# Kernel tuning notes

Measured on AMD Instinct MI355X. Metric: run time of the kernel, lower is better.

## Reference

```python
import jax, jax.numpy as jnp
import numpy as np

B, S, E, H = 2, 1024, 4096, 16
D = E // H          # head_dim = 256
RD = 64             # rotary_dim
# Quantization scales (alpha of the int8 GEMM epilogues)
A_QKV = 1.2e-4      # W8A8B8O8 q/k/v projection output scale
A_QK = 2e-4         # BMM_S8T_S8N_F32T alpha (= q_scale * k_scale)
A_PV = 1.0 / 127.0  # BMM_S8T_S8N_S8T alpha (probs quantized by *127)
A_O = 0.01          # W8A8BFP32OFP32 out_proj alpha


def setup_inputs() -> dict:
    key = jax.random.key(0)
    ks = jax.random.split(key, 9)
    ri = lambda k, shp: jax.random.randint(k, shp, -127, 128).astype(jnp.float32)
    return {
        "hidden_states": ri(ks[0], (B, S, E)),   # int8-valued activations
        "Wq": ri(ks[1], (E, E)),
        "Wk": ri(ks[2], (E, E)),
        "Wv": ri(ks[3], (E, E)),
        "Wo": ri(ks[4], (E, E)),
        "bq": ri(ks[5], (E,)),
        "bk": ri(ks[6], (E,)),
        "bv": ri(ks[7], (E,)),
        "bo": jax.random.normal(ks[8], (E,), dtype=jnp.float32) * 0.02,  # fp32 bias
    }


def _linear_i8(x, W, b, alpha):
    # W8A8B8O8Linear: int8 GEMM, scaled, +int8 bias, round+saturate to int8
    y = alpha * (x @ W.T) + b
    return jnp.clip(jnp.round(y), -128, 127)


def _rotate_every_two(x):
    x1 = x[..., ::2]
    x2 = x[..., 1::2]
    return jnp.stack((-x2, x1), axis=-1).reshape(x.shape)


def _apply_rotary(x, sin, cos):
    # duplicate_interleave == repeat each column twice; broadcast over [B, S, H, rd]
    sin = jnp.repeat(sin, 2, axis=-1)[None, :, None, :]
    cos = jnp.repeat(cos, 2, axis=-1)[None, :, None, :]
    r = x * cos + _rotate_every_two(x) * sin
    # torch: clamp(-128,127).to(int8) -> truncate toward zero
    return jnp.trunc(jnp.clip(r, -128.0, 127.0))


def reference(hidden_states, Wq, Wk, Wv, Wo, bq, bk, bv, bo):
    q = _linear_i8(hidden_states, Wq, bq, A_QKV).reshape(B, S, H, D)
    k = _linear_i8(hidden_states, Wk, bk, A_QKV).reshape(B, S, H, D)
    v = _linear_i8(hidden_states, Wv, bv, A_QKV).reshape(B, S, H, D)
    v = v.transpose(0, 2, 1, 3)  # [B, H, S, D]

    # fixed_pos_embedding over rotary_dim
    inv_freq = 1.0 / (10000.0 ** (jnp.arange(0, RD, 2, dtype=jnp.float32) / RD))
    t = jnp.arange(S, dtype=jnp.float32)
    sinusoid = t[:, None] * inv_freq[None, :]   # [S, RD/2]
    sin, cos = jnp.sin(sinusoid), jnp.cos(sinusoid)

    q = jnp.concatenate([_apply_rotary(q[..., :RD], sin, cos), q[..., RD:]], axis=-1)
    k = jnp.concatenate([_apply_rotary(k[..., :RD], sin, cos), k[..., RD:]], axis=-1)
    q = q.transpose(0, 2, 1, 3)  # [B, H, S, D]
    k = k.transpose(0, 2, 1, 3)

    w = A_QK * jnp.einsum('bhqd,bhkd->bhqk', q, k)
    causal = jnp.tril(jnp.ones((S, S), dtype=bool))[None, None]
    w = jnp.where(causal, w, jnp.finfo(jnp.float32).min)
    w = w / jnp.sqrt(jnp.float32(D))  # scale_attn = sqrt(head_dim)
    p = jnp.round(jax.nn.softmax(w, axis=-1) * 127.0)  # int8-valued probs

    # pv_bmm: int8 probs x int8 values -> scaled, round+saturate to int8
    o = jnp.clip(jnp.round(A_PV * jnp.einsum('bhqk,bhkd->bhqd', p, v)), -128, 127)
    o = o.transpose(0, 2, 1, 3).reshape(B, S, E)  # merge heads

    # out_proj: W8A8BFP32OFP32 -> fp32 output
    return A_O * (o @ Wo.T) + bo
```

## Files before the change

### kernel.cpp

```cpp
#include <hip/hip_runtime.h>
#include <hip/hip_bf16.h>

typedef int int32x4 __attribute__((ext_vector_type(4)));
typedef signed char i8;

#define B_ 2
#define S_ 1024
#define E_ 4096
#define H_ 16
#define D_ 256

#define MFMA_I8(a, b, c) __builtin_amdgcn_mfma_i32_16x16x64_i8((a), (b), (c), 0, 0, 0)

__device__ __forceinline__ int32x4 ld16(const void* p) {
    return *reinterpret_cast<const int32x4*>(p);
}

__device__ __forceinline__ void gload16(const void* g, void* l) {
    __builtin_amdgcn_global_load_lds(
        (const __attribute__((address_space(1))) void*)g,
        (__attribute__((address_space(3))) void*)l, 16, 0, 0);
}

__global__ void k_f32_to_i8(const float* __restrict__ src, i8* __restrict__ dst, int n16) {
    int i = blockIdx.x * blockDim.x + threadIdx.x;
    if (i >= n16) return;
    const float4* s = reinterpret_cast<const float4*>(src) + (size_t)i * 4;
    union { int32x4 v; i8 b[16]; } u;
#pragma unroll
    for (int j = 0; j < 4; ++j) {
        float4 f = s[j];
        u.b[j*4+0] = (i8)f.x; u.b[j*4+1] = (i8)f.y;
        u.b[j*4+2] = (i8)f.z; u.b[j*4+3] = (i8)f.w;
    }
    reinterpret_cast<int32x4*>(dst)[i] = u.v;
}

__global__ void k_sincos(float* __restrict__ sin_t, float* __restrict__ cos_t) {
    int idx = blockIdx.x * blockDim.x + threadIdx.x;
    if (idx >= S_ * 32) return;
    int s = idx >> 5, i = idx & 31;
    float ex = (float)(2 * i) / 64.0f;
    float invf = 1.0f / powf(10000.0f, ex);
    float arg = (float)s * invf;
    sin_t[idx] = (float)sin((double)arg);
    cos_t[idx] = (float)cos((double)arg);
}

template<bool OUT_I8>
__global__ __launch_bounds__(256) void k_gemm_i8(
    const i8* __restrict__ X, const i8* __restrict__ W, const float* __restrict__ bias,
    void* __restrict__ out, float alpha, int M, int N, int K)
{
    __shared__ __align__(16) i8 Alds[128 * 128];
    __shared__ __align__(16) i8 Blds[128 * 128];
    const int m0 = blockIdx.y * 128, n0 = blockIdx.x * 128;
    const int tid = threadIdx.x, lane = tid & 63, wave = tid >> 6;
    const int wr = wave >> 1, wc = wave & 1, l4 = lane & 15, lh = lane >> 4;

    int32x4 acc[4][4];
#pragma unroll
    for (int m = 0; m < 4; ++m)
#pragma unroll
        for (int n = 0; n < 4; ++n) acc[m][n] = int32x4{0, 0, 0, 0};

    for (int k0 = 0; k0 < K; k0 += 128) {
#pragma unroll
        for (int p = 0; p < 4; ++p) {
            int o = wave * 1024 + p * 4096 + lane * 16;
            int row = o >> 7, col = o & 127;
            int lb = wave * 1024 + p * 4096;
            gload16(X + (size_t)(m0 + row) * K + k0 + col, Alds + lb);
            gload16(W + (size_t)(n0 + row) * K + k0 + col, Blds + lb);
        }
        __syncthreads();
#pragma unroll
        for (int kk = 0; kk < 2; ++kk) {
            const int ko = kk * 64 + lh * 16;
            int32x4 a[4], b[4];
#pragma unroll
            for (int i = 0; i < 4; ++i) a[i] = ld16(Alds + (wr * 64 + i * 16 + l4) * 128 + ko);
#pragma unroll
            for (int i = 0; i < 4; ++i) b[i] = ld16(Blds + (wc * 64 + i * 16 + l4) * 128 + ko);
#pragma unroll
            for (int m = 0; m < 4; ++m)
#pragma unroll
                for (int n = 0; n < 4; ++n)
                    acc[m][n] = MFMA_I8(a[m], b[n], acc[m][n]);
        }
        __syncthreads();
    }

#pragma unroll
    for (int m = 0; m < 4; ++m)
#pragma unroll
        for (int n = 0; n < 4; ++n)
#pragma unroll
            for (int r = 0; r < 4; ++r) {
                int grow = m0 + wr * 64 + m * 16 + lh * 4 + r;
                int gcol = n0 + wc * 64 + n * 16 + l4;
                float y = alpha * (float)acc[m][n][r] + bias[gcol];
                if (OUT_I8) {
                    float v = rintf(y);
                    v = fminf(fmaxf(v, -128.0f), 127.0f);
                    reinterpret_cast<i8*>(out)[(size_t)grow * N + gcol] = (i8)v;
                } else {
                    reinterpret_cast<float*>(out)[(size_t)grow * N + gcol] = y;
                }
            }
}

__global__ void k_rope(const i8* __restrict__ qin, const i8* __restrict__ kin,
                       i8* __restrict__ qout, i8* __restrict__ kout,
                       const float* __restrict__ sin_t, const float* __restrict__ cos_t)
{
    const i8* in = blockIdx.y ? kin : qin;
    i8* outp = blockIdx.y ? kout : qout;
    int row = blockIdx.x * 2 + (threadIdx.x >> 7);
    int i = threadIdx.x & 127;
    int b = row / (S_ * H_);
    int s = (row / H_) % S_;
    int h = row % H_;
    const i8* src = in + (size_t)row * D_ + i * 2;
    i8 x1 = src[0], x2 = src[1];
    i8 o1, o2;
    if (i < 32) {
        float c = cos_t[s * 32 + i], sn = sin_t[s * 32 + i];
        float f1 = (float)x1, f2 = (float)x2;
        float r0 = __fadd_rn(__fmul_rn(f1, c), __fmul_rn(-f2, sn));
        float r1 = __fadd_rn(__fmul_rn(f2, c), __fmul_rn(f1, sn));
        r0 = truncf(fminf(fmaxf(r0, -128.0f), 127.0f));
        r1 = truncf(fminf(fmaxf(r1, -128.0f), 127.0f));
        o1 = (i8)r0; o2 = (i8)r1;
    } else { o1 = x1; o2 = x2; }
    size_t ob = ((size_t)(b * H_ + h) * S_ + s) * D_ + i * 2;
    outp[ob] = o1; outp[ob + 1] = o2;
}

__global__ void k_vtrans(const i8* __restrict__ vin, i8* __restrict__ vout) {
    __shared__ int tile[64][17];
    int bh = blockIdx.z;
    int b = bh >> 4, h = bh & 15;
    int s0 = blockIdx.x * 64, d0 = blockIdx.y * 64;
    int t = threadIdx.x;
    {
        int sr = t >> 2, dq = (t & 3) * 16;
        int32x4 v = ld16(vin + ((size_t)(b * S_ + s0 + sr) * H_ + h) * D_ + d0 + dq);
#pragma unroll
        for (int j = 0; j < 4; ++j) tile[sr][dq / 4 + j] = v[j];
    }
    __syncthreads();
    {
        int dr = t >> 2, sq = (t & 3) * 16;
        union { int32x4 v; i8 b[16]; } u;
        const i8* tb = reinterpret_cast<const i8*>(tile);
#pragma unroll
        for (int j = 0; j < 16; ++j) u.b[j] = tb[(sq + j) * 68 + dr];
        *reinterpret_cast<int32x4*>(vout + ((size_t)bh * D_ + d0 + dr) * S_ + s0 + sq) = u.v;
    }
}

struct AttnShared {
    float slx[4][32];
    float r127[32];
    __align__(16) i8 plds[32][80];
};

__device__ __forceinline__ void attn_chunk(int qc, int bh, int tid,
    const i8* __restrict__ Qh, const i8* __restrict__ Kb, const i8* __restrict__ Vb,
    i8* __restrict__ O, AttnShared& sh)
{
    const float C2 = 1.25e-5f * 1.44269504088896f;
    const float APV = 1.0f / 127.0f;
    const int lane = tid & 63, wave = tid >> 6;
    const int l4 = lane & 15, lh = lane >> 4;
    const i8* Qb = Qh + (size_t)(qc * 32) * D_;
    const int nt = (qc * 32 + 31) / 64 + 1;

    int32x4 aq[2][4];
#pragma unroll
    for (int m = 0; m < 2; ++m)
#pragma unroll
        for (int kk = 0; kk < 4; ++kk)
            aq[m][kk] = ld16(Qb + (size_t)(m * 16 + l4) * D_ + kk * 64 + lh * 16);

    float sum_[2][4];
#pragma unroll
    for (int m = 0; m < 2; ++m)
#pragma unroll
        for (int r = 0; r < 4; ++r) sum_[m][r] = 0.0f;

    for (int kt = 0; kt < nt; ++kt) {
        int cb = kt * 64 + wave * 16;
        int32x4 acc0 = int32x4{0,0,0,0}, acc1 = int32x4{0,0,0,0};
#pragma unroll
        for (int kk = 0; kk < 4; ++kk) {
            int32x4 bf = ld16(Kb + (size_t)(cb + l4) * D_ + kk * 64 + lh * 16);
            acc0 = MFMA_I8(aq[0][kk], bf, acc0);
            acc1 = MFMA_I8(aq[1][kk], bf, acc1);
        }
        int gcol = cb + l4;
#pragma unroll
        for (int m = 0; m < 2; ++m) {
            int32x4 accm = m ? acc1 : acc0;
#pragma unroll
            for (int r = 0; r < 4; ++r) {
                int grow = qc * 32 + m * 16 + lh * 4 + r;
                float e = (gcol <= grow) ? exp2f((float)accm[r] * C2) : 0.0f;
                sum_[m][r] += e;
            }
        }
    }

#pragma unroll
    for (int m = 0; m < 2; ++m)
#pragma unroll
        for (int r = 0; r < 4; ++r) {
            float s = sum_[m][r];
            s += __shfl_xor(s, 1);
            s += __shfl_xor(s, 2);
            s += __shfl_xor(s, 4);
            s += __shfl_xor(s, 8);
            if (l4 == 0) sh.slx[wave][m * 16 + lh * 4 + r] = s;
        }
    __syncthreads();
    if (tid < 32)
        sh.r127[tid] = 127.0f /
            (sh.slx[0][tid] + sh.slx[1][tid] + sh.slx[2][tid] + sh.slx[3][tid]);
    __syncthreads();

    int32x4 oacc[2][4];
#pragma unroll
    for (int m = 0; m < 2; ++m)
#pragma unroll
        for (int n = 0; n < 4; ++n) oacc[m][n] = int32x4{0, 0, 0, 0};

    for (int kt = 0; kt < nt; ++kt) {
        int cb = kt * 64 + wave * 16;
        int32x4 acc0 = int32x4{0,0,0,0}, acc1 = int32x4{0,0,0,0};
#pragma unroll
        for (int kk = 0; kk < 4; ++kk) {
            int32x4 bf = ld16(Kb + (size_t)(cb + l4) * D_ + kk * 64 + lh * 16);
            acc0 = MFMA_I8(aq[0][kk], bf, acc0);
            acc1 = MFMA_I8(aq[1][kk], bf, acc1);
        }
        int gcol = cb + l4;
        i8 pv[2][4];
#pragma unroll
        for (int m = 0; m < 2; ++m) {
            int32x4 accm = m ? acc1 : acc0;
#pragma unroll
            for (int r = 0; r < 4; ++r) {
                int rowi = m * 16 + lh * 4 + r;
                int grow = qc * 32 + rowi;
                float e = (gcol <= grow) ? exp2f((float)accm[r] * C2) : 0.0f;
                pv[m][r] = (i8)(int)rintf(e * sh.r127[rowi]);
            }
        }
        __syncthreads();
#pragma unroll
        for (int m = 0; m < 2; ++m)
#pragma unroll
            for (int r = 0; r < 4; ++r)
                sh.plds[m * 16 + lh * 4 + r][wave * 16 + l4] = pv[m][r];
        __syncthreads();
        int32x4 a0 = ld16(&sh.plds[l4][lh * 16]);
        int32x4 a1 = ld16(&sh.plds[16 + l4][lh * 16]);
#pragma unroll
        for (int n = 0; n < 4; ++n) {
            int32x4 bf = ld16(Vb + (size_t)(wave * 64 + n * 16 + l4) * S_ + kt * 64 + lh * 16);
            oacc[0][n] = MFMA_I8(a0, bf, oacc[0][n]);
            oacc[1][n] = MFMA_I8(a1, bf, oacc[1][n]);
        }
    }

    int b = bh >> 4, h = bh & 15;
#pragma unroll
    for (int m = 0; m < 2; ++m)
#pragma unroll
        for (int r = 0; r < 4; ++r) {
            int s = qc * 32 + m * 16 + lh * 4 + r;
#pragma unroll
            for (int n = 0; n < 4; ++n) {
                float o = rintf(APV * (float)oacc[m][n][r]);
                o = fminf(fmaxf(o, -128.0f), 127.0f);
                O[((size_t)(b * S_ + s) * H_ + h) * D_ + wave * 64 + n * 16 + l4] = (i8)o;
            }
        }
}

__global__ __launch_bounds__(256) void k_attn(const i8* __restrict__ Q, const i8* __restrict__ K,
                                              const i8* __restrict__ V, i8* __restrict__ O)
{
    __shared__ AttnShared sh;
    int bh = blockIdx.x;
    int p = blockIdx.y;
    int tid = threadIdx.x;
    const i8* Qh = Q + (size_t)bh * S_ * D_;
    const i8* Kb = K + (size_t)bh * S_ * D_;
    const i8* Vb = V + (size_t)bh * D_ * S_;
    attn_chunk((S_ / 32 - 1) - p, bh, tid, Qh, Kb, Vb, O, sh);
    attn_chunk(p, bh, tid, Qh, Kb, Vb, O, sh);
}

extern "C" void kernel_launch(void* const* d_in, const int* in_sizes, int n_in,
                              void* d_out, int out_size, void* d_ws, size_t ws_size,
                              hipStream_t stream) {
    const float* hs = (const float*)d_in[0];
    const float* Wq = (const float*)d_in[1];
    const float* Wk = (const float*)d_in[2];
    const float* Wv = (const float*)d_in[3];
    const float* Wo = (const float*)d_in[4];
    const float* bq = (const float*)d_in[5];
    const float* bk = (const float*)d_in[6];
    const float* bv = (const float*)d_in[7];
    const float* bo = (const float*)d_in[8];
    float* out = (float*)d_out;

    size_t off = 0;
    char* wsb = (char*)d_ws;
    auto carve = [&](size_t bytes) { char* p = wsb + off; off += (bytes + 255) & ~(size_t)255; return p; };
    const size_t ME = (size_t)B_ * S_ * E_;
    const size_t EE = (size_t)E_ * E_;
    i8* x8  = (i8*)carve(ME);
    i8* wq8 = (i8*)carve(EE);
    i8* wk8 = (i8*)carve(EE);
    i8* wv8 = (i8*)carve(EE);
    i8* wo8 = (i8*)carve(EE);
    i8* q8  = (i8*)carve(ME);
    i8* k8  = (i8*)carve(ME);
    i8* v8  = (i8*)carve(ME);
    i8* qr  = (i8*)carve(ME);
    i8* kr  = (i8*)carve(ME);
    i8* vt  = (i8*)carve(ME);
    i8* o8  = (i8*)carve(ME);
    float* sin_t = (float*)carve((size_t)S_ * 32 * 4);
    float* cos_t = (float*)carve((size_t)S_ * 32 * 4);

    int n16_me = (int)(ME / 16), n16_ee = (int)(EE / 16);
    k_f32_to_i8<<<(n16_me + 255) / 256, 256, 0, stream>>>(hs, x8, n16_me);
    k_f32_to_i8<<<(n16_ee + 255) / 256, 256, 0, stream>>>(Wq, wq8, n16_ee);
    k_f32_to_i8<<<(n16_ee + 255) / 256, 256, 0, stream>>>(Wk, wk8, n16_ee);
    k_f32_to_i8<<<(n16_ee + 255) / 256, 256, 0, stream>>>(Wv, wv8, n16_ee);
    k_f32_to_i8<<<(n16_ee + 255) / 256, 256, 0, stream>>>(Wo, wo8, n16_ee);
    k_sincos<<<(S_ * 32 + 255) / 256, 256, 0, stream>>>(sin_t, cos_t);

    const int M = B_ * S_, N = E_, Kd = E_;
    dim3 gg(N / 128, M / 128);
    k_gemm_i8<true><<<gg, 256, 0, stream>>>(x8, wq8, bq, q8, 0.00012f, M, N, Kd);
    k_gemm_i8<true><<<gg, 256, 0, stream>>>(x8, wk8, bk, k8, 0.00012f, M, N, Kd);
    k_gemm_i8<true><<<gg, 256, 0, stream>>>(x8, wv8, bv, v8, 0.00012f, M, N, Kd);

    k_rope<<<dim3((B_ * S_ * H_) / 2, 2), 256, 0, stream>>>(q8, k8, qr, kr, sin_t, cos_t);
    k_vtrans<<<dim3(S_ / 64, D_ / 64, B_ * H_), 256, 0, stream>>>(v8, vt);
    k_attn<<<dim3(B_ * H_, S_ / 64), 256, 0, stream>>>(qr, kr, vt, o8);

    k_gemm_i8<false><<<gg, 256, 0, stream>>>(o8, wo8, bo, out, 0.01f, M, N, Kd);
}
```

Before: 363.0 us.

## Triple-buffer int8 GEMM with swizzled LDS, XCD-aware tile mapping, fused weight casts

The int8 GEMM changes from a single-buffered K=128 loop to a 3-stage K=64 ring of LDS buffers. Global-to-LDS loads for tile t+2 are issued between the MFMA halves of tile t, guarded by vmcnt/lgkmcnt waits and barriers, with s_setprio raised around the MFMA bursts. LDS columns are XOR-swizzled to cut bank conflicts, and a 1D grid is remapped so consecutive tiles land on the same XCD for L2 reuse. The four weight casts are merged into one launch; the extra barriers and hand-written waitcnts add sync overhead and risk correctness if the counts are wrong.

```diff
diff --git a/kernel.cpp b/kernel.cpp
--- a/kernel.cpp
+++ b/kernel.cpp
@@ -22,9 +22,33 @@
         (__attribute__((address_space(3))) void*)l, 16, 0, 0);
 }
 
+#define WAIT_VM4()  asm volatile("s_waitcnt vmcnt(4)" ::: "memory")
+#define WAIT_VM0()  asm volatile("s_waitcnt vmcnt(0)" ::: "memory")
+#define WAIT_LGKM0() do { asm volatile("s_waitcnt lgkmcnt(0)" ::: "memory"); \
+                          __builtin_amdgcn_sched_barrier(0); } while (0)
+
 __global__ void k_f32_to_i8(const float* __restrict__ src, i8* __restrict__ dst, int n16) {
     int i = blockIdx.x * blockDim.x + threadIdx.x;
     if (i >= n16) return;
+    const float4* s = reinterpret_cast<const float4*>(src) + (size_t)i * 4;
+    union { int32x4 v; i8 b[16]; } u;
+#pragma unroll
+    for (int j = 0; j < 4; ++j) {
+        float4 f = s[j];
+        u.b[j*4+0] = (i8)f.x; u.b[j*4+1] = (i8)f.y;
+        u.b[j*4+2] = (i8)f.z; u.b[j*4+3] = (i8)f.w;
+    }
+    reinterpret_cast<int32x4*>(dst)[i] = u.v;
+}
+
+__global__ void k_w_to_i8(const float* __restrict__ w0, const float* __restrict__ w1,
+                          const float* __restrict__ w2, const float* __restrict__ w3,
+                          i8* __restrict__ d0, i8* __restrict__ d1,
+                          i8* __restrict__ d2, i8* __restrict__ d3, int n16) {
+    int i = blockIdx.x * blockDim.x + threadIdx.x;
+    if (i >= n16) return;
+    const float* src = (blockIdx.y == 0) ? w0 : (blockIdx.y == 1) ? w1 : (blockIdx.y == 2) ? w2 : w3;
+    i8* dst = (blockIdx.y == 0) ? d0 : (blockIdx.y == 1) ? d1 : (blockIdx.y == 2) ? d2 : d3;
     const float4* s = reinterpret_cast<const float4*>(src) + (size_t)i * 4;
     union { int32x4 v; i8 b[16]; } u;
 #pragma unroll
@@ -52,44 +76,88 @@
     const i8* __restrict__ X, const i8* __restrict__ W, const float* __restrict__ bias,
     void* __restrict__ out, float alpha, int M, int N, int K)
 {
-    __shared__ __align__(16) i8 Alds[128 * 128];
-    __shared__ __align__(16) i8 Blds[128 * 128];
-    const int m0 = blockIdx.y * 128, n0 = blockIdx.x * 128;
+    __shared__ __align__(16) i8 Alds[3][8192];
+    __shared__ __align__(16) i8 Blds[3][8192];
+    const int nt = K >> 6;
+    const int nwg = (M >> 7) * (N >> 7);
+    const int q = nwg >> 3;
+    const int lin = blockIdx.x;
+    const int wg = (lin & 7) * q + (lin >> 3);
+    const int nbm = M >> 7;
+    const int m0 = (wg % nbm) * 128, n0 = (wg / nbm) * 128;
+
     const int tid = threadIdx.x, lane = tid & 63, wave = tid >> 6;
     const int wr = wave >> 1, wc = wave & 1, l4 = lane & 15, lh = lane >> 4;
 
+    const int g4 = lh ^ ((l4 >> 1) & 3);
+    const int aoff = (wr * 64 + l4) * 64 + g4 * 16;
+    const int boff = (wc * 64 + l4) * 64 + g4 * 16;
+
+    const int srow = tid >> 2;
+    const int sg = (tid & 3) ^ ((tid >> 3) & 3);
+    const i8* Asrc = X + (size_t)(m0 + srow) * K + sg * 16;
+    const i8* Bsrc = W + (size_t)(n0 + srow) * K + sg * 16;
+    const size_t rstep = (size_t)64 * K;
+    const int ldst = wave * 1024;
+
+#define STAGE_A(t_) do { int kb_ = (t_) * 64; i8* lb_ = Alds[(t_) % 3];      \
+        gload16(Asrc + kb_,         lb_ + ldst);                             \
+        gload16(Asrc + rstep + kb_, lb_ + 4096 + ldst); } while (0)
+#define STAGE_B(t_) do { int kb_ = (t_) * 64; i8* lb_ = Blds[(t_) % 3];      \
+        gload16(Bsrc + kb_,         lb_ + ldst);                             \
+        gload16(Bsrc + rstep + kb_, lb_ + 4096 + ldst); } while (0)
+
     int32x4 acc[4][4];
 #pragma unroll
     for (int m = 0; m < 4; ++m)
 #pragma unroll
         for (int n = 0; n < 4; ++n) acc[m][n] = int32x4{0, 0, 0, 0};
 
-    for (int k0 = 0; k0 < K; k0 += 128) {
-#pragma unroll
-        for (int p = 0; p < 4; ++p) {
-            int o = wave * 1024 + p * 4096 + lane * 16;
-            int row = o >> 7, col = o & 127;
-            int lb = wave * 1024 + p * 4096;
-            gload16(X + (size_t)(m0 + row) * K + k0 + col, Alds + lb);
-            gload16(W + (size_t)(n0 + row) * K + k0 + col, Blds + lb);
-        }
-        __syncthreads();
-#pragma unroll
-        for (int kk = 0; kk < 2; ++kk) {
-            const int ko = kk * 64 + lh * 16;
-            int32x4 a[4], b[4];
-#pragma unroll
-            for (int i = 0; i < 4; ++i) a[i] = ld16(Alds + (wr * 64 + i * 16 + l4) * 128 + ko);
-#pragma unroll
-            for (int i = 0; i < 4; ++i) b[i] = ld16(Blds + (wc * 64 + i * 16 + l4) * 128 + ko);
-#pragma unroll
-            for (int m = 0; m < 4; ++m)
-#pragma unroll
-                for (int n = 0; n < 4; ++n)
-                    acc[m][n] = MFMA_I8(a[m], b[n], acc[m][n]);
-        }
-        __syncthreads();
-    }
+    STAGE_A(0); STAGE_B(0);
+    STAGE_A(1); STAGE_B(1);
+
+    for (int t = 0; t < nt; ++t) {
+        const i8* Ab = Alds[t % 3];
+        const i8* Bb = Blds[t % 3];
+        if (t + 1 < nt) { WAIT_VM4(); } else { WAIT_VM0(); }
+        __builtin_amdgcn_s_barrier();
+
+        int32x4 a0, a1, a2, a3, b0, b1, b2, b3;
+        a0 = ld16(Ab + aoff);        a1 = ld16(Ab + aoff + 1024);
+        a2 = ld16(Ab + aoff + 2048); a3 = ld16(Ab + aoff + 3072);
+        b0 = ld16(Bb + boff);        b1 = ld16(Bb + boff + 1024);
+        if (t + 2 < nt) STAGE_A(t + 2);
+        __builtin_amdgcn_s_barrier();
+        WAIT_LGKM0();
+        __builtin_amdgcn_s_setprio(1);
+        acc[0][0] = MFMA_I8(a0, b0, acc[0][0]);
+        acc[1][0] = MFMA_I8(a1, b0, acc[1][0]);
+        acc[2][0] = MFMA_I8(a2, b0, acc[2][0]);
+        acc[3][0] = MFMA_I8(a3, b0, acc[3][0]);
+        acc[0][1] = MFMA_I8(a0, b1, acc[0][1]);
+        acc[1][1] = MFMA_I8(a1, b1, acc[1][1]);
+        acc[2][1] = MFMA_I8(a2, b1, acc[2][1]);
+        acc[3][1] = MFMA_I8(a3, b1, acc[3][1]);
+        __builtin_amdgcn_s_setprio(0);
+        __builtin_amdgcn_s_barrier();
+
+        b2 = ld16(Bb + boff + 2048); b3 = ld16(Bb + boff + 3072);
+        if (t + 2 < nt) STAGE_B(t + 2);
+        __builtin_amdgcn_s_barrier();
+        WAIT_LGKM0();
+        __builtin_amdgcn_s_setprio(1);
+        acc[0][2] = MFMA_I8(a0, b2, acc[0][2]);
+        acc[1][2] = MFMA_I8(a1, b2, acc[1][2]);
+        acc[2][2] = MFMA_I8(a2, b2, acc[2][2]);
+        acc[3][2] = MFMA_I8(a3, b2, acc[3][2]);
+        acc[0][3] = MFMA_I8(a0, b3, acc[0][3]);
+        acc[1][3] = MFMA_I8(a1, b3, acc[1][3]);
+        acc[2][3] = MFMA_I8(a2, b3, acc[2][3]);
+        acc[3][3] = MFMA_I8(a3, b3, acc[3][3]);
+        __builtin_amdgcn_s_setprio(0);
+    }
+#undef STAGE_A
+#undef STAGE_B
 
 #pragma unroll
     for (int m = 0; m < 4; ++m)
@@ -339,21 +407,19 @@
 
     int n16_me = (int)(ME / 16), n16_ee = (int)(EE / 16);
     k_f32_to_i8<<<(n16_me + 255) / 256, 256, 0, stream>>>(hs, x8, n16_me);
-    k_f32_to_i8<<<(n16_ee + 255) / 256, 256, 0, stream>>>(Wq, wq8, n16_ee);
-    k_f32_to_i8<<<(n16_ee + 255) / 256, 256, 0, stream>>>(Wk, wk8, n16_ee);
-    k_f32_to_i8<<<(n16_ee + 255) / 256, 256, 0, stream>>>(Wv, wv8, n16_ee);
-    k_f32_to_i8<<<(n16_ee + 255) / 256, 256, 0, stream>>>(Wo, wo8, n16_ee);
+    k_w_to_i8<<<dim3((n16_ee + 255) / 256, 4), 256, 0, stream>>>(
+        Wq, Wk, Wv, Wo, wq8, wk8, wv8, wo8, n16_ee);
     k_sincos<<<(S_ * 32 + 255) / 256, 256, 0, stream>>>(sin_t, cos_t);
 
     const int M = B_ * S_, N = E_, Kd = E_;
-    dim3 gg(N / 128, M / 128);
-    k_gemm_i8<true><<<gg, 256, 0, stream>>>(x8, wq8, bq, q8, 0.00012f, M, N, Kd);
-    k_gemm_i8<true><<<gg, 256, 0, stream>>>(x8, wk8, bk, k8, 0.00012f, M, N, Kd);
-    k_gemm_i8<true><<<gg, 256, 0, stream>>>(x8, wv8, bv, v8, 0.00012f, M, N, Kd);
+    const int nwg = (M / 128) * (N / 128);
+    k_gemm_i8<true><<<nwg, 256, 0, stream>>>(x8, wq8, bq, q8, 0.00012f, M, N, Kd);
+    k_gemm_i8<true><<<nwg, 256, 0, stream>>>(x8, wk8, bk, k8, 0.00012f, M, N, Kd);
+    k_gemm_i8<true><<<nwg, 256, 0, stream>>>(x8, wv8, bv, v8, 0.00012f, M, N, Kd);
 
     k_rope<<<dim3((B_ * S_ * H_) / 2, 2), 256, 0, stream>>>(q8, k8, qr, kr, sin_t, cos_t);
     k_vtrans<<<dim3(S_ / 64, D_ / 64, B_ * H_), 256, 0, stream>>>(v8, vt);
     k_attn<<<dim3(B_ * H_, S_ / 64), 256, 0, stream>>>(qr, kr, vt, o8);
 
-    k_gemm_i8<false><<<gg, 256, 0, stream>>>(o8, wo8, bo, out, 0.01f, M, N, Kd);
-}
+    k_gemm_i8<false><<<nwg, 256, 0, stream>>>(o8, wo8, bo, out, 0.01f, M, N, Kd);
+}
```

Result: faster. 331.3 us (-8.8%).
